# Kernel tuning notes

Measured on AMD Instinct MI355X. Metric: run time of the kernel, lower is better.

Reference implementation:

```python
import jax, jax.numpy as jnp
from jax import lax
import numpy as np

LN_EPS = 1e-5

def layernorm(x, g, b):
    m = jnp.mean(x, axis=-1, keepdims=True)
    v = jnp.mean((x - m) ** 2, axis=-1, keepdims=True)
    return (x - m) / jnp.sqrt(v + LN_EPS) * g + b

def setup_inputs() -> dict:
    key = jax.random.key(0)
    ks = jax.random.split(key, 16)
    B, C, T = 64, 8, 2048
    K, L = 128, 64
    E, NC = 64, 10
    s = 0.05
    d = {}
    d["x"] = jax.random.normal(ks[0], (B, C, T), jnp.float32)
    d["shapelets"] = jax.random.uniform(ks[1], (K, C, L), jnp.float32, -1.0, 1.0)
    # local encoder: Linear(K->E) + LayerNorm
    d["w_loc"] = jax.random.normal(ks[2], (K, E), jnp.float32) * s
    d["b_loc"] = jnp.zeros((E,), jnp.float32)
    d["g_loc"] = jnp.ones((E,), jnp.float32)
    d["be_loc"] = jnp.zeros((E,), jnp.float32)
    # global conv: Conv2d(1->16,(3,5)) , Conv2d(16->32,(3,5))
    d["conv1_w"] = jax.random.normal(ks[3], (16, 1, 3, 5), jnp.float32) * s
    d["conv1_b"] = jnp.zeros((16,), jnp.float32)
    d["conv2_w"] = jax.random.normal(ks[4], (32, 16, 3, 5), jnp.float32) * s
    d["conv2_b"] = jnp.zeros((32,), jnp.float32)
    # global encoder: Linear(32->E) + LayerNorm
    d["w_glob"] = jax.random.normal(ks[5], (32, E), jnp.float32) * s
    d["b_glob"] = jnp.zeros((E,), jnp.float32)
    d["g_glob"] = jnp.ones((E,), jnp.float32)
    d["be_glob"] = jnp.zeros((E,), jnp.float32)
    # MultiheadAttention (torch layout): in_proj (3E,E), out_proj (E,E)
    d["in_proj_w"] = jax.random.normal(ks[6], (3 * E, E), jnp.float32) * s
    d["in_proj_b"] = jnp.zeros((3 * E,), jnp.float32)
    d["out_w"] = jax.random.normal(ks[7], (E, E), jnp.float32) * s
    d["out_b"] = jnp.zeros((E,), jnp.float32)
    # MLP head: Linear(E->E//2), Linear(E//2->NC)
    d["mlp_w1"] = jax.random.normal(ks[8], (E, E // 2), jnp.float32) * s
    d["mlp_b1"] = jnp.zeros((E // 2,), jnp.float32)
    d["mlp_w2"] = jax.random.normal(ks[9], (E // 2, NC), jnp.float32) * s
    d["mlp_b2"] = jnp.zeros((NC,), jnp.float32)
    return d

def reference(x, shapelets, w_loc, b_loc, g_loc, be_loc,
              conv1_w, conv1_b, conv2_w, conv2_b,
              w_glob, b_glob, g_glob, be_glob,
              in_proj_w, in_proj_b, out_w, out_b,
              mlp_w1, mlp_b1, mlp_w2, mlp_b2):
    B, C, T = x.shape
    K, _, L = shapelets.shape
    n_heads = 8
    # ---- shapelet min squared distance via ||w||^2 - 2*corr + ||s||^2 ----
    # corr: (B, K, W) with W = T - L + 1; same math as the unfold/broadcast version
    corr = lax.conv_general_dilated(x, shapelets, (1,), 'VALID',
                                    dimension_numbers=('NCH', 'OIH', 'NCH'))
    win_sq = lax.conv_general_dilated(x * x, jnp.ones((1, C, L), x.dtype), (1,), 'VALID',
                                      dimension_numbers=('NCH', 'OIH', 'NCH'))  # (B,1,W)
    s_sq = jnp.sum(shapelets * shapelets, axis=(1, 2))  # (K,)
    dist_sq = win_sq - 2.0 * corr + s_sq[None, :, None]  # (B,K,W)
    feat = jnp.min(dist_sq, axis=2)  # (B,K)
    # ---- local encoder ----
    local = layernorm(jax.nn.relu(feat @ w_loc + b_loc), g_loc, be_loc)  # (B,E)
    # ---- global conv branch on (B,1,C,T) ----
    h = x[:, None, :, :]
    h = lax.conv_general_dilated(h, conv1_w, (1, 1), [(1, 1), (2, 2)],
                                 dimension_numbers=('NCHW', 'OIHW', 'NCHW'))
    h = jax.nn.relu(h + conv1_b[None, :, None, None])
    h = lax.reduce_window(h, -jnp.inf, lax.max, (1, 1, 1, 2), (1, 1, 1, 2), 'VALID')
    h = lax.conv_general_dilated(h, conv2_w, (1, 1), [(1, 1), (2, 2)],
                                 dimension_numbers=('NCHW', 'OIHW', 'NCHW'))
    h = jax.nn.relu(h + conv2_b[None, :, None, None])
    h = lax.reduce_window(h, -jnp.inf, lax.max, (1, 1, 1, 2), (1, 1, 1, 2), 'VALID')
    g = jnp.mean(h, axis=(2, 3))  # AdaptiveAvgPool2d((1,1)) + Flatten -> (B,32)
    glob = layernorm(jax.nn.relu(g @ w_glob + b_glob), g_glob, be_glob)  # (B,E)
    # ---- cross attention (query len 1, kv len 1) ----
    E = local.shape[-1]
    hd = E // n_heads
    wq, wk, wv = jnp.split(in_proj_w, 3, axis=0)
    bq, bk, bv = jnp.split(in_proj_b, 3)
    q = (local @ wq.T + bq).reshape(B, n_heads, hd)
    k = (glob @ wk.T + bk).reshape(B, n_heads, hd)
    v = (glob @ wv.T + bv).reshape(B, n_heads, hd)
    scores = jnp.sum(q * k, axis=-1, keepdims=True) / jnp.sqrt(jnp.float32(hd))  # (B,H,1)
    attn = jax.nn.softmax(scores, axis=-1)  # kv length 1 -> all ones
    attn_out = (attn * v).reshape(B, E) @ out_w.T + out_b  # (B,E)
    # ---- MLP head (dropout is identity in eval) ----
    hmid = jax.nn.relu(attn_out @ mlp_w1 + mlp_b1)
    return hmid @ mlp_w2 + mlp_b2
```

## Files before the change

kernel.cpp:

```cpp
#include <hip/hip_runtime.h>
#include <math.h>


typedef __attribute__((ext_vector_type(4))) _Float16 f16x4;
typedef __attribute__((ext_vector_type(8)))  _Float16 f16x8;
typedef __attribute__((ext_vector_type(16))) float    f32x16;

#define WT 64
#define NT 16
#define H1_OFF   0
#define XS_OFF   21760
#define LDS_BYTES 26368

template <int CTRL>
__device__ __forceinline__ float dppf(float v) {
    return __uint_as_float(__builtin_amdgcn_update_dpp(
        0u, __float_as_uint(v), CTRL, 0xF, 0xF, true));
}
#define DPP_XOR1 0xB1
#define DPP_XOR2 0x4E
#define DPP_ROR4 0x124
#define DPP_ROR8 0x128

__global__ void prep_frags(const float* __restrict__ w2, _Float16* __restrict__ fragg) {
    const int t    = blockIdx.x;
    const int lane = threadIdx.x;
    const int kh   = t / 5, kw = t - kh * 5;
    const int oc   = lane & 31;
    const int ic0  = (lane >> 5) * 8;
    f16x8 hv;
    #pragma unroll
    for (int j = 0; j < 8; ++j)
        hv[j] = (_Float16)w2[((oc * 16 + ic0 + j) * 3 + kh) * 5 + kw];
    *(f16x8*)&fragg[(t * 64 + lane) * 8] = hv;
}

__global__ __launch_bounds__(256, 4) void conv_fused(
    const float* __restrict__ x,
    const float* __restrict__ w1, const float* __restrict__ b1,
    const float* __restrict__ b2,
    const _Float16* __restrict__ fragg,
    float* __restrict__ part)
{
    const int wt  = blockIdx.x;
    const int b   = blockIdx.y;
    const int tid = threadIdx.x;
    const int w0  = wt * WT;

    __shared__ __align__(16) unsigned int ldsu[LDS_BYTES / 4];
    _Float16* h1 = (_Float16*)((char*)ldsu + H1_OFF);
    float*    xs = (float*)((char*)ldsu + XS_OFF);

    const int q = tid & 3;
    float wreg[60];
    float bias1[4];
    #pragma unroll
    for (int j = 0; j < 4; ++j) {
        #pragma unroll
        for (int k = 0; k < 15; ++k) wreg[j * 15 + k] = w1[(q * 4 + j) * 15 + k];
        bias1[j] = b1[q * 4 + j];
    }

    const int t0 = 2 * w0 - 6;
    for (int i = tid; i < 8 * 144; i += 256) {
        int r = i / 144, tl = i - r * 144;
        int t = t0 + tl;
        float v = 0.f;
        if (tl < 140 && t >= 0 && t < 2048) v = x[(b * 8 + r) * 2048 + t];
        xs[i] = v;
    }
    {
        unsigned int* hh = (unsigned int*)h1;
        for (int i = tid; i < 544; i += 256) {
            hh[i] = 0u; hh[4896 + i] = 0u;
        }
    }
    __syncthreads();

    #pragma unroll
    for (int pass = 0; pass < 3; ++pass) {
        if (pass == 2 && tid >= 32) break;
        const int idx = (tid >> 2) + pass * 64;
        const int r   = idx / 17;
        const int c4  = idx - r * 17;
        const int cb  = c4 * 8;
        float xv[3][12];
        #pragma unroll
        for (int pq = 0; pq < 3; ++pq) {
            int rr = r + pq - 1;
            if (rr >= 0 && rr < 8) {
                const float4* p = (const float4*)&xs[rr * 144 + cb];
                float4 a0 = p[0], a1 = p[1], a2 = p[2];
                xv[pq][0]=a0.x; xv[pq][1]=a0.y; xv[pq][2]=a0.z; xv[pq][3]=a0.w;
                xv[pq][4]=a1.x; xv[pq][5]=a1.y; xv[pq][6]=a1.z; xv[pq][7]=a1.w;
                xv[pq][8]=a2.x; xv[pq][9]=a2.y; xv[pq][10]=a2.z; xv[pq][11]=a2.w;
            } else {
                #pragma unroll
                for (int z = 0; z < 12; ++z) xv[pq][z] = 0.f;
            }
        }
        #pragma unroll
        for (int cc = 0; cc < 4; ++cc) {
            const int wc = w0 - 2 + 4 * c4 + cc;
            f16x4 hv;
            #pragma unroll
            for (int j = 0; j < 4; ++j) {
                float c0 = bias1[j], c1 = bias1[j];
                #pragma unroll
                for (int kh = 0; kh < 3; ++kh)
                    #pragma unroll
                    for (int kw = 0; kw < 5; ++kw) {
                        float wgt = wreg[j * 15 + kh * 5 + kw];
                        c0 = fmaf(xv[kh][2 * cc + kw],     wgt, c0);
                        c1 = fmaf(xv[kh][2 * cc + kw + 1], wgt, c1);
                    }
                float v = fmaxf(fmaxf(c0, c1), 0.f);
                if (wc < 0 || wc >= 1024) v = 0.f;
                hv[j] = (_Float16)v;
            }
            *(f16x4*)&h1[((r + 1) * 68 + 4 * c4 + cc) * 16 + q * 4] = hv;
        }
    }
    __syncthreads();

    const int lane  = tid & 63;
    const int wave  = tid >> 6;
    const int laneN = lane & 31;
    const int icoff = (lane >> 5) * 8;
    const int half  = lane >> 5;

    f32x16 acc[4];
    #pragma unroll
    for (int nt = 0; nt < 4; ++nt)
        #pragma unroll
        for (int r = 0; r < 16; ++r) acc[nt][r] = 0.f;

    const f16x8* Ag = (const f16x8*)fragg;
    f16x8 a_cur = Ag[lane];
    for (int t = 0; t < 15; ++t) {
        f16x8 a_nxt = (t < 14) ? Ag[(t + 1) * 64 + lane] : a_cur;
        int kh = t / 5, kw = t - kh * 5;
        #pragma unroll
        for (int nt = 0; nt < 4; ++nt) {
            int hrow = 2 * wave + (nt >> 1);
            int wn0  = (nt & 1) * 32;
            int idx  = ((hrow + kh) * 68 + wn0 + laneN + kw) * 16 + icoff;
            f16x8 bv = *(const f16x8*)&h1[idx];
            acc[nt] = __builtin_amdgcn_mfma_f32_32x32x16_f16(a_cur, bv, acc[nt], 0, 0, 0);
        }
        a_cur = a_nxt;
    }

    float b2v[16], sums[16];
    #pragma unroll
    for (int r = 0; r < 16; ++r) {
        b2v[r]  = b2[(r & 3) + 8 * (r >> 2) + 4 * half];
        sums[r] = 0.f;
    }
    #pragma unroll
    for (int nt = 0; nt < 4; ++nt)
        #pragma unroll
        for (int r = 0; r < 16; ++r) {
            float d = acc[nt][r] + b2v[r];
            float o = fmaxf(fmaxf(d, dppf<DPP_XOR1>(d)), 0.f);
            sums[r] += o;
        }
    #pragma unroll
    for (int r = 0; r < 16; ++r) {
        float s = sums[r];
        s += dppf<DPP_XOR1>(s);
        s += dppf<DPP_XOR2>(s);
        s += dppf<DPP_ROR4>(s);
        s += dppf<DPP_ROR8>(s);
        sums[r] = s;
    }
    if ((lane & 15) == 0) {
        const int nh = (lane >> 4) & 1;
        #pragma unroll
        for (int r = 0; r < 16; ++r) {
            int oc = (r & 3) + 8 * (r >> 2) + 4 * half;
            part[((b * 32 + oc) * 16 + wt) * 8 + wave * 2 + nh] = 0.5f * sums[r];
        }
    }
}

__global__ void tail_kernel(
    const float* __restrict__ part,
    const float* __restrict__ w_glob, const float* __restrict__ b_glob,
    const float* __restrict__ g_glob, const float* __restrict__ be_glob,
    const float* __restrict__ in_proj_w, const float* __restrict__ in_proj_b,
    const float* __restrict__ out_w, const float* __restrict__ out_b,
    const float* __restrict__ mlp_w1, const float* __restrict__ mlp_b1,
    const float* __restrict__ mlp_w2, const float* __restrict__ mlp_b2,
    float* __restrict__ out)
{
    const int b = blockIdx.x;
    const int e = threadIdx.x;
    __shared__ float gs[32], glob_s[64], vs[64], aos[64], hms[32];

    if (e < 32) {
        float sm = 0.f;
        #pragma unroll
        for (int t = 0; t < 128; ++t) sm += part[(b * 32 + e) * 128 + t];
        gs[e] = sm * (1.f / 4096.f);
    }
    __syncthreads();

    float acc = b_glob[e];
    #pragma unroll
    for (int i = 0; i < 32; ++i) acc = fmaf(gs[i], w_glob[i * 64 + e], acc);
    acc = fmaxf(acc, 0.f);

    float m = acc;
    #pragma unroll
    for (int k = 32; k >= 1; k >>= 1) m += __shfl_xor(m, k);
    m *= (1.f / 64.f);
    float d = acc - m;
    float vv = d * d;
    #pragma unroll
    for (int k = 32; k >= 1; k >>= 1) vv += __shfl_xor(vv, k);
    vv *= (1.f / 64.f);
    float gl = d * (1.f / sqrtf(vv + 1e-5f)) * g_glob[e] + be_glob[e];
    glob_s[e] = gl;
    __syncthreads();

    float vval = in_proj_b[128 + e];
    #pragma unroll
    for (int j = 0; j < 64; ++j) vval = fmaf(glob_s[j], in_proj_w[(128 + e) * 64 + j], vval);
    vs[e] = vval;
    __syncthreads();

    float ao = out_b[e];
    #pragma unroll
    for (int j = 0; j < 64; ++j) ao = fmaf(vs[j], out_w[e * 64 + j], ao);
    aos[e] = ao;
    __syncthreads();

    if (e < 32) {
        float hm = mlp_b1[e];
        #pragma unroll
        for (int j = 0; j < 64; ++j) hm = fmaf(aos[j], mlp_w1[j * 32 + e], hm);
        hms[e] = fmaxf(hm, 0.f);
    }
    __syncthreads();

    if (e < 10) {
        float o = mlp_b2[e];
        #pragma unroll
        for (int i = 0; i < 32; ++i) o = fmaf(hms[i], mlp_w2[i * 10 + e], o);
        out[b * 10 + e] = o;
    }
}

extern "C" void kernel_launch(void* const* d_in, const int* in_sizes, int n_in,
                              void* d_out, int out_size, void* d_ws, size_t ws_size,
                              hipStream_t stream) {
    const float* x        = (const float*)d_in[0];
    const float* conv1_w  = (const float*)d_in[6];
    const float* conv1_b  = (const float*)d_in[7];
    const float* conv2_w  = (const float*)d_in[8];
    const float* conv2_b  = (const float*)d_in[9];
    const float* w_glob   = (const float*)d_in[10];
    const float* b_glob   = (const float*)d_in[11];
    const float* g_glob   = (const float*)d_in[12];
    const float* be_glob  = (const float*)d_in[13];
    const float* in_proj_w = (const float*)d_in[14];
    const float* in_proj_b = (const float*)d_in[15];
    const float* out_w    = (const float*)d_in[16];
    const float* out_b    = (const float*)d_in[17];
    const float* mlp_w1   = (const float*)d_in[18];
    const float* mlp_b1   = (const float*)d_in[19];
    const float* mlp_w2   = (const float*)d_in[20];
    const float* mlp_b2   = (const float*)d_in[21];

    _Float16* fragg = (_Float16*)d_ws;
    float* partials = (float*)((char*)d_ws + 15360);

    prep_frags<<<15, 64, 0, stream>>>(conv2_w, fragg);

    dim3 grid(NT, 64);
    conv_fused<<<grid, 256, 0, stream>>>(x, conv1_w, conv1_b, conv2_b, fragg, partials);

    tail_kernel<<<64, 64, 0, stream>>>(partials, w_glob, b_glob, g_glob, be_glob,
                                       in_proj_w, in_proj_b, out_w, out_b,
                                       mlp_w1, mlp_b1, mlp_w2, mlp_b2,
                                       (float*)d_out);
}
```

Baseline: 125.2 us.

## Fuse weight prep and tail MLP into conv kernel via atomic last-block reduction

Removes the separate weight-fragment prep kernel and tail kernel. The conv kernel now loads conv2 weights directly from global memory and converts them to fp16 per wave. Per-batch partial sums are accumulated with float atomics, and the last block per batch, found through an atomic counter, runs the global encoder, attention and MLP head using wave shuffles. This trades two launches for a memset, scattered strided weight loads inside the MFMA loop, atomic contention and non-deterministic summation order.

```diff
diff --git a/kernel.cpp b/kernel.cpp
--- a/kernel.cpp
+++ b/kernel.cpp
@@ -22,25 +22,19 @@
 #define DPP_ROR4 0x124
 #define DPP_ROR8 0x128
 
-__global__ void prep_frags(const float* __restrict__ w2, _Float16* __restrict__ fragg) {
-    const int t    = blockIdx.x;
-    const int lane = threadIdx.x;
-    const int kh   = t / 5, kw = t - kh * 5;
-    const int oc   = lane & 31;
-    const int ic0  = (lane >> 5) * 8;
-    f16x8 hv;
-    #pragma unroll
-    for (int j = 0; j < 8; ++j)
-        hv[j] = (_Float16)w2[((oc * 16 + ic0 + j) * 3 + kh) * 5 + kw];
-    *(f16x8*)&fragg[(t * 64 + lane) * 8] = hv;
-}
-
 __global__ __launch_bounds__(256, 4) void conv_fused(
     const float* __restrict__ x,
     const float* __restrict__ w1, const float* __restrict__ b1,
-    const float* __restrict__ b2,
-    const _Float16* __restrict__ fragg,
-    float* __restrict__ part)
+    const float* __restrict__ w2, const float* __restrict__ b2,
+    const float* __restrict__ w_glob, const float* __restrict__ b_glob,
+    const float* __restrict__ g_glob, const float* __restrict__ be_glob,
+    const float* __restrict__ in_proj_w, const float* __restrict__ in_proj_b,
+    const float* __restrict__ out_w, const float* __restrict__ out_b,
+    const float* __restrict__ mlp_w1, const float* __restrict__ mlp_b1,
+    const float* __restrict__ mlp_w2, const float* __restrict__ mlp_b2,
+    float* __restrict__ gacc,
+    int*   __restrict__ cnt,
+    float* __restrict__ out)
 {
     const int wt  = blockIdx.x;
     const int b   = blockIdx.y;
@@ -48,6 +42,7 @@
     const int w0  = wt * WT;
 
     __shared__ __align__(16) unsigned int ldsu[LDS_BYTES / 4];
+    __shared__ int lastf;
     _Float16* h1 = (_Float16*)((char*)ldsu + H1_OFF);
     float*    xs = (float*)((char*)ldsu + XS_OFF);
 
@@ -135,11 +130,26 @@
         #pragma unroll
         for (int r = 0; r < 16; ++r) acc[nt][r] = 0.f;
 
-    const f16x8* Ag = (const f16x8*)fragg;
-    f16x8 a_cur = Ag[lane];
+    f16x8 a_cur;
+    {
+        float af[8];
+        #pragma unroll
+        for (int j = 0; j < 8; ++j)
+            af[j] = w2[((laneN * 16 + icoff + j) * 3 + 0) * 5 + 0];
+        #pragma unroll
+        for (int j = 0; j < 8; ++j) a_cur[j] = (_Float16)af[j];
+    }
+
     for (int t = 0; t < 15; ++t) {
-        f16x8 a_nxt = (t < 14) ? Ag[(t + 1) * 64 + lane] : a_cur;
-        int kh = t / 5, kw = t - kh * 5;
+        const int kh = t / 5, kw = t - kh * 5;
+        float anf[8];
+        if (t < 14) {
+            const int t1  = t + 1;
+            const int kh1 = t1 / 5, kw1 = t1 - kh1 * 5;
+            #pragma unroll
+            for (int j = 0; j < 8; ++j)
+                anf[j] = w2[((laneN * 16 + icoff + j) * 3 + kh1) * 5 + kw1];
+        }
         #pragma unroll
         for (int nt = 0; nt < 4; ++nt) {
             int hrow = 2 * wave + (nt >> 1);
@@ -148,7 +158,12 @@
             f16x8 bv = *(const f16x8*)&h1[idx];
             acc[nt] = __builtin_amdgcn_mfma_f32_32x32x16_f16(a_cur, bv, acc[nt], 0, 0, 0);
         }
-        a_cur = a_nxt;
+        if (t < 14) {
+            f16x8 an;
+            #pragma unroll
+            for (int j = 0; j < 8; ++j) an[j] = (_Float16)anf[j];
+            a_cur = an;
+        }
     }
 
     float b2v[16], sums[16];
@@ -175,81 +190,58 @@
         sums[r] = s;
     }
     if ((lane & 15) == 0) {
-        const int nh = (lane >> 4) & 1;
         #pragma unroll
         for (int r = 0; r < 16; ++r) {
             int oc = (r & 3) + 8 * (r >> 2) + 4 * half;
-            part[((b * 32 + oc) * 16 + wt) * 8 + wave * 2 + nh] = 0.5f * sums[r];
-        }
-    }
-}
-
-__global__ void tail_kernel(
-    const float* __restrict__ part,
-    const float* __restrict__ w_glob, const float* __restrict__ b_glob,
-    const float* __restrict__ g_glob, const float* __restrict__ be_glob,
-    const float* __restrict__ in_proj_w, const float* __restrict__ in_proj_b,
-    const float* __restrict__ out_w, const float* __restrict__ out_b,
-    const float* __restrict__ mlp_w1, const float* __restrict__ mlp_b1,
-    const float* __restrict__ mlp_w2, const float* __restrict__ mlp_b2,
-    float* __restrict__ out)
-{
-    const int b = blockIdx.x;
-    const int e = threadIdx.x;
-    __shared__ float gs[32], glob_s[64], vs[64], aos[64], hms[32];
-
-    if (e < 32) {
-        float sm = 0.f;
-        #pragma unroll
-        for (int t = 0; t < 128; ++t) sm += part[(b * 32 + e) * 128 + t];
-        gs[e] = sm * (1.f / 4096.f);
-    }
-    __syncthreads();
-
-    float acc = b_glob[e];
-    #pragma unroll
-    for (int i = 0; i < 32; ++i) acc = fmaf(gs[i], w_glob[i * 64 + e], acc);
-    acc = fmaxf(acc, 0.f);
-
-    float m = acc;
+            atomicAdd(&gacc[b * 32 + oc], 0.5f * sums[r]);
+        }
+    }
+
+    __threadfence();
+    __syncthreads();
+    if (tid == 0) lastf = (atomicAdd(&cnt[b], 1) == NT - 1) ? 1 : 0;
+    __syncthreads();
+    if (!lastf || tid >= 64) return;
+    __threadfence();
+
+    const int e  = tid;
+    const int eo = e & 31;
+    float gval = gacc[b * 32 + eo] * (1.f / 4096.f);
+
+    float accv = b_glob[e];
+    #pragma unroll
+    for (int i = 0; i < 32; ++i) accv = fmaf(__shfl(gval, i), w_glob[i * 64 + e], accv);
+    accv = fmaxf(accv, 0.f);
+
+    float m = accv;
     #pragma unroll
     for (int k = 32; k >= 1; k >>= 1) m += __shfl_xor(m, k);
     m *= (1.f / 64.f);
-    float d = acc - m;
-    float vv = d * d;
+    float dd = accv - m;
+    float vv = dd * dd;
     #pragma unroll
     for (int k = 32; k >= 1; k >>= 1) vv += __shfl_xor(vv, k);
     vv *= (1.f / 64.f);
-    float gl = d * (1.f / sqrtf(vv + 1e-5f)) * g_glob[e] + be_glob[e];
-    glob_s[e] = gl;
-    __syncthreads();
+    float gl = dd * (1.f / sqrtf(vv + 1e-5f)) * g_glob[e] + be_glob[e];
 
     float vval = in_proj_b[128 + e];
-    #pragma unroll
-    for (int j = 0; j < 64; ++j) vval = fmaf(glob_s[j], in_proj_w[(128 + e) * 64 + j], vval);
-    vs[e] = vval;
-    __syncthreads();
+    #pragma unroll 16
+    for (int j = 0; j < 64; ++j) vval = fmaf(__shfl(gl, j), in_proj_w[(128 + e) * 64 + j], vval);
 
     float ao = out_b[e];
-    #pragma unroll
-    for (int j = 0; j < 64; ++j) ao = fmaf(vs[j], out_w[e * 64 + j], ao);
-    aos[e] = ao;
-    __syncthreads();
-
-    if (e < 32) {
-        float hm = mlp_b1[e];
-        #pragma unroll
-        for (int j = 0; j < 64; ++j) hm = fmaf(aos[j], mlp_w1[j * 32 + e], hm);
-        hms[e] = fmaxf(hm, 0.f);
-    }
-    __syncthreads();
-
-    if (e < 10) {
-        float o = mlp_b2[e];
-        #pragma unroll
-        for (int i = 0; i < 32; ++i) o = fmaf(hms[i], mlp_w2[i * 10 + e], o);
-        out[b * 10 + e] = o;
-    }
+    #pragma unroll 16
+    for (int j = 0; j < 64; ++j) ao = fmaf(__shfl(vval, j), out_w[e * 64 + j], ao);
+
+    float hm = mlp_b1[eo];
+    #pragma unroll 16
+    for (int j = 0; j < 64; ++j) hm = fmaf(__shfl(ao, j), mlp_w1[j * 32 + eo], hm);
+    hm = fmaxf(hm, 0.f);
+
+    const int ee = (e < 10) ? e : 0;
+    float o = mlp_b2[ee];
+    #pragma unroll
+    for (int i = 0; i < 32; ++i) o = fmaf(__shfl(hm, i), mlp_w2[i * 10 + ee], o);
+    if (e < 10) out[b * 10 + e] = o;
 }
 
 extern "C" void kernel_launch(void* const* d_in, const int* in_sizes, int n_in,
@@ -273,16 +265,15 @@
     const float* mlp_w2   = (const float*)d_in[20];
     const float* mlp_b2   = (const float*)d_in[21];
 
-    _Float16* fragg = (_Float16*)d_ws;
-    float* partials = (float*)((char*)d_ws + 15360);
-
-    prep_frags<<<15, 64, 0, stream>>>(conv2_w, fragg);
+    float* gacc = (float*)d_ws;
+    int*   cnt  = (int*)((char*)d_ws + 8192);
+
+    hipMemsetAsync(d_ws, 0, 8192 + 256, stream);
 
     dim3 grid(NT, 64);
-    conv_fused<<<grid, 256, 0, stream>>>(x, conv1_w, conv1_b, conv2_b, fragg, partials);
-
-    tail_kernel<<<64, 64, 0, stream>>>(partials, w_glob, b_glob, g_glob, be_glob,
-                                       in_proj_w, in_proj_b, out_w, out_b,
-                                       mlp_w1, mlp_b1, mlp_w2, mlp_b2,
-                                       (float*)d_out);
+    conv_fused<<<grid, 256, 0, stream>>>(x, conv1_w, conv1_b, conv2_w, conv2_b,
+                                         w_glob, b_glob, g_glob, be_glob,
+                                         in_proj_w, in_proj_b, out_w, out_b,
+                                         mlp_w1, mlp_b1, mlp_w2, mlp_b2,
+                                         gacc, cnt, (float*)d_out);
 }
```

After: 303.7 us. +142.6%, slower.
